# Performance work log

Hardware: AMD Instinct MI355X
Metric: run time of the kernel (lower is better)

## Reference

```python
import jax, jax.numpy as jnp
import numpy as np

L, B, IN, H, OUT = 4, 4096, 1024, 1024, 1024


def setup_inputs() -> dict:
    key = jax.random.key(0)
    ks = jax.random.split(key, 9)
    std = 1.0 / (H + IN) ** 0.5
    return {
        "x": jax.random.normal(ks[0], (B, IN), jnp.float32),
        "h_prev": jax.random.normal(ks[1], (L, B, H), jnp.float32),
        "c_prev": jax.random.normal(ks[2], (L, B, H), jnp.float32),
        "Wi": jax.random.uniform(ks[3], (L, IN, 4 * H), jnp.float32, -std, std),
        "Wh": jax.random.uniform(ks[4], (L, H, 4 * H), jnp.float32, -std, std),
        "bi": jax.random.uniform(ks[5], (L, 4 * H), jnp.float32, -std, std),
        "bh": jax.random.uniform(ks[6], (L, 4 * H), jnp.float32, -std, std),
        "fc_W": jax.random.uniform(ks[7], (H, OUT), jnp.float32, -std, std),
        "fc_b": jax.random.uniform(ks[8], (OUT,), jnp.float32, -std, std),
    }


def _lstm_cell(x, h, c, Wi, Wh, bi, bh):
    # gates: [B, 4H], split into (input, forget, cell, output)
    gates = x @ Wi + bi + h @ Wh + bh
    i, f, g, o = jnp.split(gates, 4, axis=1)
    i, f, o = jax.nn.sigmoid(i), jax.nn.sigmoid(f), jax.nn.sigmoid(o)
    g = jnp.tanh(g)
    c_cur = f * c + i * g
    h_cur = o * jnp.tanh(c_cur)
    return h_cur, c_cur


def reference(x, h_prev, c_prev, Wi, Wh, bi, bh, fc_W, fc_b):
    h_out, c_out = [], []
    x_in = x
    for l in range(L):  # fixed small layer loop
        h_cur, c_cur = _lstm_cell(x_in, h_prev[l], c_prev[l], Wi[l], Wh[l], bi[l], bh[l])
        h_out.append(h_cur)
        c_out.append(c_cur)
        x_in = h_cur
    h_out = jnp.stack(h_out, axis=0)
    c_out = jnp.stack(c_out, axis=0)
    y = h_out[-1] @ fc_W + fc_b
    return y, h_out, c_out
```

## Files before the change

kernel.cpp:

```cpp
#include <hip/hip_runtime.h>

#define B_    4096
#define H_    1024
#define NLAY  4
#define NK    32
#define NT512 512

typedef __attribute__((ext_vector_type(8))) short bf16x8;
typedef __attribute__((ext_vector_type(4))) float f32x4;
typedef unsigned short ushort_t;

__device__ __forceinline__ ushort_t f2bf(float f) {
  unsigned u = __builtin_bit_cast(unsigned, f);
  u += 0x7FFFu + ((u >> 16) & 1u);
  return (ushort_t)(u >> 16);
}

__device__ __forceinline__ float fast_sigmoid(float x) {
  float e = __expf(-fabsf(x));
  float s = 1.0f / (1.0f + e);
  return x >= 0.0f ? s : 1.0f - s;
}
__device__ __forceinline__ float fast_tanh(float x) {
  float e = __expf(-2.0f * fabsf(x));
  float t = (1.0f - e) / (1.0f + e);
  return x >= 0.0f ? t : -t;
}

#define GLDS16(gsrc, ldst)                                                  \
  __builtin_amdgcn_global_load_lds(                                         \
      (__attribute__((address_space(1))) void*)(gsrc),                      \
      (__attribute__((address_space(3))) void*)(ldst), 16, 0, 0)

#define BAR()                                                               \
  { asm volatile("" ::: "memory");                                          \
    __builtin_amdgcn_s_barrier();                                           \
    asm volatile("" ::: "memory"); }

#define WAITV(N)                                                            \
  { asm volatile("s_waitcnt vmcnt(" #N ")" ::: "memory");                   \
    __builtin_amdgcn_sched_barrier(0); }

__global__ __launch_bounds__(NT512, 2) void lstm8(
    const ushort_t* __restrict__ aX, const ushort_t* __restrict__ aH,
    const float* __restrict__ cprev, const float* __restrict__ bi,
    const float* __restrict__ bh, const ushort_t* __restrict__ wt,
    float* __restrict__ hout, float* __restrict__ cout,
    ushort_t* __restrict__ hbfout) {
  __shared__ __align__(16) char sL[131072];

  const int tid  = threadIdx.x;
  const int lane = tid & 63;
  const int wid  = tid >> 6;
  const int wm   = wid >> 2;
  const int wn   = wid & 3;
  const int bid  = (blockIdx.x & 7) * 32 + (blockIdx.x >> 3);
  const int bm   = bid & 15;
  const int bn   = bid >> 4;

  const int fr    = lane & 15;
  const int oF    = lane >> 4;
  const int s_    = oF ^ ((fr >> 1) & 3);
  const int aBase = (wm * 128 + fr) * 64 + s_ * 16;
  const int bBase = (wn * 64 + fr) * 64 + s_ * 16;

  const int rA = tid >> 2;
  const int oA = (tid & 3) ^ ((rA >> 1) & 3);
  const size_t aOff = (size_t)(bm * 256 + rA) * 1024 + oA * 8;

  f32x4 acc[8][4];
#pragma unroll
  for (int m = 0; m < 8; ++m)
#pragma unroll
    for (int g = 0; g < 4; ++g) acc[m][g] = (f32x4){0.f, 0.f, 0.f, 0.f};

#define STAGE_A(nb, kt, kh)                                                  \
  {                                                                          \
    const ushort_t* s0 =                                                     \
        (((kt) < 16) ? aX : aH) + aOff + ((kt) & 15) * 64 + (kh) * 32;       \
    GLDS16(s0, sL + (nb)*65536 + (kh)*16384 + wid * 1024);                   \
    GLDS16(s0 + 131072, sL + (nb)*65536 + (kh)*16384 + 8192 + wid * 1024);   \
  }
#define STAGE_B(nb, kt, kh)                                                  \
  {                                                                          \
    const ushort_t* s0 =                                                     \
        wt + ((size_t)(bn * 32 + (kt))) * 16384 + (kh)*8192 + tid * 8;       \
    GLDS16(s0, sL + (nb)*65536 + 32768 + (kh)*16384 + wid * 1024);           \
    GLDS16(s0 + 4096,                                                        \
           sL + (nb)*65536 + 32768 + (kh)*16384 + 8192 + wid * 1024);        \
  }

  STAGE_A(0, 0, 0);
  STAGE_B(0, 0, 0);
  STAGE_A(0, 0, 1);
  STAGE_B(0, 0, 1);
  WAITV(4);
  BAR();

#pragma unroll 1
  for (int kt = 0; kt < NK; ++kt) {
    const int cb = kt & 1, nb = cb ^ 1;
    const bool st = (kt + 1 < NK);
    const char* pa = sL + cb * 65536;
    const char* pb = sL + cb * 65536 + 32768;

    bf16x8 a[8], bb0, bb1;
#pragma unroll
    for (int m = 0; m < 8; ++m)
      a[m] = *(const bf16x8*)(pa + aBase + m * 1024);
    bb0 = *(const bf16x8*)(pb + bBase);
    bb1 = *(const bf16x8*)(pb + bBase + 1024);
    if (st) STAGE_A(nb, kt + 1, 0);
    BAR();
    __builtin_amdgcn_s_setprio(1);
#pragma unroll
    for (int m = 0; m < 8; ++m)
      acc[m][0] = __builtin_amdgcn_mfma_f32_16x16x32_bf16(a[m], bb0, acc[m][0], 0, 0, 0);
#pragma unroll
    for (int m = 0; m < 8; ++m)
      acc[m][1] = __builtin_amdgcn_mfma_f32_16x16x32_bf16(a[m], bb1, acc[m][1], 0, 0, 0);
    __builtin_amdgcn_s_setprio(0);
    BAR();
    bb0 = *(const bf16x8*)(pb + bBase + 2048);
    bb1 = *(const bf16x8*)(pb + bBase + 3072);
    if (st) STAGE_B(nb, kt + 1, 0);
    BAR();
    __builtin_amdgcn_s_setprio(1);
#pragma unroll
    for (int m = 0; m < 8; ++m)
      acc[m][2] = __builtin_amdgcn_mfma_f32_16x16x32_bf16(a[m], bb0, acc[m][2], 0, 0, 0);
#pragma unroll
    for (int m = 0; m < 8; ++m)
      acc[m][3] = __builtin_amdgcn_mfma_f32_16x16x32_bf16(a[m], bb1, acc[m][3], 0, 0, 0);
    __builtin_amdgcn_s_setprio(0);
    if (st) { WAITV(4); } else { WAITV(0); }
    BAR();
#pragma unroll
    for (int m = 0; m < 8; ++m)
      a[m] = *(const bf16x8*)(pa + 16384 + aBase + m * 1024);
    bb0 = *(const bf16x8*)(pb + 16384 + bBase);
    bb1 = *(const bf16x8*)(pb + 16384 + bBase + 1024);
    if (st) STAGE_A(nb, kt + 1, 1);
    BAR();
    __builtin_amdgcn_s_setprio(1);
#pragma unroll
    for (int m = 0; m < 8; ++m)
      acc[m][0] = __builtin_amdgcn_mfma_f32_16x16x32_bf16(a[m], bb0, acc[m][0], 0, 0, 0);
#pragma unroll
    for (int m = 0; m < 8; ++m)
      acc[m][1] = __builtin_amdgcn_mfma_f32_16x16x32_bf16(a[m], bb1, acc[m][1], 0, 0, 0);
    __builtin_amdgcn_s_setprio(0);
    BAR();
    bb0 = *(const bf16x8*)(pb + 16384 + bBase + 2048);
    bb1 = *(const bf16x8*)(pb + 16384 + bBase + 3072);
    if (st) STAGE_B(nb, kt + 1, 1);
    BAR();
    __builtin_amdgcn_s_setprio(1);
#pragma unroll
    for (int m = 0; m < 8; ++m)
      acc[m][2] = __builtin_amdgcn_mfma_f32_16x16x32_bf16(a[m], bb0, acc[m][2], 0, 0, 0);
#pragma unroll
    for (int m = 0; m < 8; ++m)
      acc[m][3] = __builtin_amdgcn_mfma_f32_16x16x32_bf16(a[m], bb1, acc[m][3], 0, 0, 0);
    __builtin_amdgcn_s_setprio(0);
    if (st) { WAITV(4); }
    BAR();
  }
#undef STAGE_A
#undef STAGE_B

  const int hcol = bn * 64 + wn * 16 + fr;
  float bsum[4];
#pragma unroll
  for (int g = 0; g < 4; ++g)
    bsum[g] = bi[g * 1024 + hcol] + bh[g * 1024 + hcol];
#pragma unroll
  for (int m = 0; m < 8; ++m) {
    const int row0 = bm * 256 + wm * 128 + m * 16 + (lane >> 4) * 4;
#pragma unroll
    for (int r = 0; r < 4; ++r) {
      const int row = row0 + r;
      const float gi = fast_sigmoid(acc[m][0][r] + bsum[0]);
      const float gf = fast_sigmoid(acc[m][1][r] + bsum[1]);
      const float gg = fast_tanh(acc[m][2][r] + bsum[2]);
      const float go = fast_sigmoid(acc[m][3][r] + bsum[3]);
      const float cp = cprev[(size_t)row * H_ + hcol];
      const float c  = gf * cp + gi * gg;
      const float h  = go * fast_tanh(c);
      cout[(size_t)row * H_ + hcol]   = c;
      hout[(size_t)row * H_ + hcol]   = h;
      hbfout[(size_t)row * H_ + hcol] = f2bf(h);
    }
  }
}

__global__ __launch_bounds__(NT512) void packW(const float* __restrict__ Wi,
                                               const float* __restrict__ Wh,
                                               ushort_t* __restrict__ wt) {
  __shared__ ushort_t t16[64 * 256];
  const int bn = blockIdx.x;
  const int ks = blockIdx.y;
  const int l  = blockIdx.z;
  const int tid = threadIdx.x;
  const int kq = tid >> 6, cc = tid & 63;
  const int k0 = ks * 64;
  const float* W = (k0 < 1024)
                       ? (Wi + (size_t)l * 1024 * 4096 + (size_t)k0 * 4096)
                       : (Wh + (size_t)l * 1024 * 4096 + (size_t)(k0 - 1024) * 4096);
#pragma unroll
  for (int kk = 0; kk < 8; ++kk) {
    const int kl = kq * 8 + kk;
#pragma unroll
    for (int g = 0; g < 4; ++g) {
      const float v = W[(size_t)kl * 4096 + g * 1024 + bn * 64 + cc];
      const int p = (cc >> 4) * 64 + g * 16 + (cc & 15);
      t16[kl * 256 + p] = f2bf(v);
    }
  }
  __syncthreads();
  ushort_t* tile = wt + (((size_t)l * 16 + bn) * 32 + ks) * 16384;
#pragma unroll
  for (int j = 0; j < 4; ++j) {
    const int idx = j * 512 + tid;
    const int q = idx & 1023;
    const int r = q >> 2, s = q & 3;
    const int o = s ^ ((r >> 1) & 3);
    const int kl = (idx >> 10) * 32 + o * 8;
    bf16x8 ov;
#pragma unroll
    for (int i = 0; i < 8; ++i) ov[i] = (short)t16[(kl + i) * 256 + r];
    *(bf16x8*)(tile + (size_t)idx * 8) = ov;
  }
}

__device__ __forceinline__ int swz(int row, int kelem) {
  return ((row * 64 + kelem) * 2) ^ ((row & 7) << 4);
}

__global__ __launch_bounds__(NT512) void fc_kernel(
    const ushort_t* __restrict__ wtfc, const ushort_t* __restrict__ abf,
    const float* __restrict__ bias, float* __restrict__ y) {
  __shared__ __align__(16) char sA[128 * 64 * 2];
  __shared__ __align__(16) char sB[64 * 64 * 2];
  const int tid  = threadIdx.x;
  const int lane = tid & 63;
  const int wid  = tid >> 6;
  const int wm   = wid >> 2;
  const int wn   = wid & 3;
  const int bid  = (blockIdx.x & 7) * 64 + (blockIdx.x >> 3);
  const int bm   = bid & 31;
  const int bn   = bid >> 5;

  f32x4 acc[4];
#pragma unroll
  for (int m = 0; m < 4; ++m) acc[m] = (f32x4){0.f, 0.f, 0.f, 0.f};

  const int rloc = wid * 8 + (lane >> 3);
  const int jA   = (lane & 7) ^ ((lane >> 3) & 7);
  const ushort_t* aSrc = abf + (size_t)(bm * 128 + rloc) * 1024 + jA * 8;

  for (int ks = 0; ks < 16; ++ks) {
    __syncthreads();
    GLDS16(wtfc + (size_t)(bn * 16 + ks) * 4096 + tid * 8, sB + wid * 1024);
    const int off = ks * 64;
    GLDS16(aSrc + off,             sA + wid * 1024);
    GLDS16(aSrc + off + 64 * 1024, sA + 8192 + wid * 1024);
    __syncthreads();
#pragma unroll
    for (int kk = 0; kk < 64; kk += 32) {
      const int ke = kk + (lane >> 4) * 8;
      bf16x8 a[4];
#pragma unroll
      for (int m = 0; m < 4; ++m)
        a[m] = *(const bf16x8*)(sA + swz(wm * 64 + m * 16 + (lane & 15), ke));
      bf16x8 b = *(const bf16x8*)(sB + swz(wn * 16 + (lane & 15), ke));
#pragma unroll
      for (int m = 0; m < 4; ++m)
        acc[m] = __builtin_amdgcn_mfma_f32_16x16x32_bf16(a[m], b, acc[m], 0, 0, 0);
    }
  }
  const int col = bn * 64 + wn * 16 + (lane & 15);
  const float bb = bias[col];
#pragma unroll
  for (int m = 0; m < 4; ++m) {
    const int row0 = bm * 128 + wm * 64 + m * 16 + ((lane >> 4) << 2);
#pragma unroll
    for (int r = 0; r < 4; ++r)
      y[(size_t)(row0 + r) * 1024 + col] = acc[m][r] + bb;
  }
}

__global__ __launch_bounds__(NT512) void transposeFc(const float* __restrict__ W,
                                                     ushort_t* __restrict__ wt) {
  const int bn = blockIdx.x;
  const int ks = blockIdx.y;
  const int tid = threadIdx.x;
  const int c  = tid & 63;
  const int ko = (tid >> 6) * 8;
  float v[8];
#pragma unroll
  for (int j = 0; j < 8; ++j)
    v[j] = W[(size_t)(ks * 64 + ko + j) * 1024 + bn * 64 + c];
  bf16x8 o;
#pragma unroll
  for (int j = 0; j < 8; ++j) o[j] = (short)f2bf(v[j]);
  ushort_t* tile = wt + ((size_t)bn * 16 + ks) * 4096;
  *(bf16x8*)((char*)tile + swz(c, ko)) = o;
}

__global__ __launch_bounds__(256) void cvt_bf16(const float* __restrict__ s,
                                                ushort_t* __restrict__ d,
                                                int n8) {
  const int i = blockIdx.x * 256 + threadIdx.x;
  if (i >= n8) return;
  const float* p = s + (size_t)i * 8;
  f32x4 a = ((const f32x4*)p)[0];
  f32x4 b = ((const f32x4*)p)[1];
  bf16x8 o;
#pragma unroll
  for (int j = 0; j < 4; ++j) {
    o[j]     = (short)f2bf(a[j]);
    o[4 + j] = (short)f2bf(b[j]);
  }
  *(bf16x8*)(d + (size_t)i * 8) = o;
}

extern "C" void kernel_launch(void* const* d_in, const int* in_sizes, int n_in,
                              void* d_out, int out_size, void* d_ws,
                              size_t ws_size, hipStream_t stream) {
  const float* x     = (const float*)d_in[0];
  const float* hprev = (const float*)d_in[1];
  const float* cprev = (const float*)d_in[2];
  const float* Wi    = (const float*)d_in[3];
  const float* Wh    = (const float*)d_in[4];
  const float* bi    = (const float*)d_in[5];
  const float* bh    = (const float*)d_in[6];
  const float* fcW   = (const float*)d_in[7];
  const float* fcb   = (const float*)d_in[8];

  float* out = (float*)d_out;
  const size_t BH = (size_t)B_ * H_;
  float* y    = out;
  float* hout = out + BH;
  float* cout = out + 5 * BH;

  const size_t WT_ELEMS = (size_t)4 * 16 * 32 * 16384;
  const size_t FC_ELEMS = (size_t)16 * 16 * 4096;
  ushort_t* wt      = (ushort_t*)d_ws;
  ushort_t* fcwt    = wt + WT_ELEMS;
  ushort_t* xbf     = fcwt + FC_ELEMS;
  ushort_t* hprevbf = xbf + BH;
  ushort_t* houtbf  = hprevbf + 4 * BH;

  dim3 blk(NT512);
  packW<<<dim3(16, 32, 4), blk, 0, stream>>>(Wi, Wh, wt);
  transposeFc<<<dim3(16, 16), blk, 0, stream>>>(fcW, fcwt);
  cvt_bf16<<<dim3((int)(BH / 8 / 256)), dim3(256), 0, stream>>>(x, xbf,
                                                                (int)(BH / 8));
  cvt_bf16<<<dim3((int)(4 * BH / 8 / 256)), dim3(256), 0, stream>>>(
      hprev, hprevbf, (int)(4 * BH / 8));

  for (int l = 0; l < NLAY; ++l) {
    const ushort_t* aX  = (l == 0) ? xbf : (houtbf + (size_t)(l - 1) * BH);
    const ushort_t* wtl = wt + (size_t)l * 16 * 32 * 16384;
    lstm8<<<dim3(256), blk, 0, stream>>>(
        aX, hprevbf + (size_t)l * BH, cprev + (size_t)l * BH, bi + l * 4096,
        bh + l * 4096, wtl, hout + (size_t)l * BH, cout + (size_t)l * BH,
        houtbf + (size_t)l * BH);
  }
  fc_kernel<<<dim3(512), blk, 0, stream>>>(fcwt, houtbf + 3 * BH, fcb, y);
}
```

Baseline: 434.2 us.

## Use 4-buffer 3-deep LDS pipeline and coalesce LSTM epilogue via LDS

The LSTM GEMM main loop moves from a double-buffered pipeline over 64-wide K tiles, which had several barriers per half-step, to a four-slot ring of 32-wide K tiles prefetched three steps ahead with a single wait and barrier per step. The packed weight layout is split into 8192-element half tiles to match. The epilogue now stages c_prev, c and h through LDS so global reads and writes are coalesced float4 rows, with the bf16 h copy written as 4-wide vectors. The cost is extra LDS round trips and barriers in the epilogue, and the deeper prefetch may raise register and LDS pressure.

```diff
diff --git a/kernel.cpp b/kernel.cpp
--- a/kernel.cpp
+++ b/kernel.cpp
@@ -3,10 +3,10 @@
 #define B_    4096
 #define H_    1024
 #define NLAY  4
-#define NK    32
 #define NT512 512
 
 typedef __attribute__((ext_vector_type(8))) short bf16x8;
+typedef __attribute__((ext_vector_type(4))) short s16x4;
 typedef __attribute__((ext_vector_type(4))) float f32x4;
 typedef unsigned short ushort_t;
 
@@ -68,130 +68,164 @@
   const int oA = (tid & 3) ^ ((rA >> 1) & 3);
   const size_t aOff = (size_t)(bm * 256 + rA) * 1024 + oA * 8;
 
+  const ushort_t* wtBn = wt + (size_t)bn * 64 * 8192;
+
   f32x4 acc[8][4];
 #pragma unroll
   for (int m = 0; m < 8; ++m)
 #pragma unroll
     for (int g = 0; g < 4; ++g) acc[m][g] = (f32x4){0.f, 0.f, 0.f, 0.f};
 
-#define STAGE_A(nb, kt, kh)                                                  \
+#pragma unroll
+  for (int t = 0; t < 3; ++t) {
+    const ushort_t* s0 = aX + aOff + t * 32;
+    GLDS16(s0,          sL + t * 32768 + wid * 1024);
+    GLDS16(s0 + 131072, sL + t * 32768 + 8192 + wid * 1024);
+    const ushort_t* sb = wtBn + (size_t)t * 8192 + tid * 8;
+    GLDS16(sb,        sL + t * 32768 + 16384 + wid * 1024);
+    GLDS16(sb + 4096, sL + t * 32768 + 16384 + 8192 + wid * 1024);
+  }
+  WAITV(8);
+  BAR();
+
+#define TSTEP(BUFC, T, ISSUE)                                                \
   {                                                                          \
-    const ushort_t* s0 =                                                     \
-        (((kt) < 16) ? aX : aH) + aOff + ((kt) & 15) * 64 + (kh) * 32;       \
-    GLDS16(s0, sL + (nb)*65536 + (kh)*16384 + wid * 1024);                   \
-    GLDS16(s0 + 131072, sL + (nb)*65536 + (kh)*16384 + 8192 + wid * 1024);   \
-  }
-#define STAGE_B(nb, kt, kh)                                                  \
-  {                                                                          \
-    const ushort_t* s0 =                                                     \
-        wt + ((size_t)(bn * 32 + (kt))) * 16384 + (kh)*8192 + tid * 8;       \
-    GLDS16(s0, sL + (nb)*65536 + 32768 + (kh)*16384 + wid * 1024);           \
-    GLDS16(s0 + 4096,                                                        \
-           sL + (nb)*65536 + 32768 + (kh)*16384 + 8192 + wid * 1024);        \
-  }
-
-  STAGE_A(0, 0, 0);
-  STAGE_B(0, 0, 0);
-  STAGE_A(0, 0, 1);
-  STAGE_B(0, 0, 1);
-  WAITV(4);
-  BAR();
+    const char* pa = sL + (BUFC) * 32768;                                    \
+    const char* pb = pa + 16384;                                             \
+    char* nbuf = sL + (((BUFC) + 3) & 3) * 32768;                            \
+    bf16x8 a[8], b0, b1;                                                     \
+    _Pragma("unroll")                                                        \
+    for (int m = 0; m < 8; ++m)                                              \
+      a[m] = *(const bf16x8*)(pa + aBase + m * 1024);                        \
+    b0 = *(const bf16x8*)(pb + bBase);                                       \
+    b1 = *(const bf16x8*)(pb + bBase + 1024);                                \
+    if (ISSUE) {                                                             \
+      const int tt = (T) + 3;                                                \
+      const ushort_t* s0 = (tt < 32 ? aX : aH) + (aOff + (tt & 31) * 32);    \
+      GLDS16(s0,          nbuf + wid * 1024);                                \
+      GLDS16(s0 + 131072, nbuf + 8192 + wid * 1024);                         \
+    }                                                                        \
+    __builtin_amdgcn_s_setprio(1);                                           \
+    _Pragma("unroll")                                                        \
+    for (int m = 0; m < 8; ++m)                                              \
+      acc[m][0] =                                                            \
+          __builtin_amdgcn_mfma_f32_16x16x32_bf16(a[m], b0, acc[m][0], 0, 0, 0); \
+    _Pragma("unroll")                                                        \
+    for (int m = 0; m < 8; ++m)                                              \
+      acc[m][1] =                                                            \
+          __builtin_amdgcn_mfma_f32_16x16x32_bf16(a[m], b1, acc[m][1], 0, 0, 0); \
+    __builtin_amdgcn_s_setprio(0);                                           \
+    bf16x8 b2 = *(const bf16x8*)(pb + bBase + 2048);                         \
+    bf16x8 b3 = *(const bf16x8*)(pb + bBase + 3072);                         \
+    if (ISSUE) {                                                             \
+      const int tt = (T) + 3;                                                \
+      const ushort_t* sb = wtBn + (size_t)tt * 8192 + tid * 8;               \
+      GLDS16(sb,        nbuf + 16384 + wid * 1024);                          \
+      GLDS16(sb + 4096, nbuf + 16384 + 8192 + wid * 1024);                   \
+    }                                                                        \
+    __builtin_amdgcn_s_setprio(1);                                           \
+    _Pragma("unroll")                                                        \
+    for (int m = 0; m < 8; ++m)                                              \
+      acc[m][2] =                                                            \
+          __builtin_amdgcn_mfma_f32_16x16x32_bf16(a[m], b2, acc[m][2], 0, 0, 0); \
+    _Pragma("unroll")                                                        \
+    for (int m = 0; m < 8; ++m)                                              \
+      acc[m][3] =                                                            \
+          __builtin_amdgcn_mfma_f32_16x16x32_bf16(a[m], b3, acc[m][3], 0, 0, 0); \
+    __builtin_amdgcn_s_setprio(0);                                           \
+  }
 
 #pragma unroll 1
-  for (int kt = 0; kt < NK; ++kt) {
-    const int cb = kt & 1, nb = cb ^ 1;
-    const bool st = (kt + 1 < NK);
-    const char* pa = sL + cb * 65536;
-    const char* pb = sL + cb * 65536 + 32768;
-
-    bf16x8 a[8], bb0, bb1;
-#pragma unroll
-    for (int m = 0; m < 8; ++m)
-      a[m] = *(const bf16x8*)(pa + aBase + m * 1024);
-    bb0 = *(const bf16x8*)(pb + bBase);
-    bb1 = *(const bf16x8*)(pb + bBase + 1024);
-    if (st) STAGE_A(nb, kt + 1, 0);
-    BAR();
-    __builtin_amdgcn_s_setprio(1);
-#pragma unroll
-    for (int m = 0; m < 8; ++m)
-      acc[m][0] = __builtin_amdgcn_mfma_f32_16x16x32_bf16(a[m], bb0, acc[m][0], 0, 0, 0);
-#pragma unroll
-    for (int m = 0; m < 8; ++m)
-      acc[m][1] = __builtin_amdgcn_mfma_f32_16x16x32_bf16(a[m], bb1, acc[m][1], 0, 0, 0);
-    __builtin_amdgcn_s_setprio(0);
-    BAR();
-    bb0 = *(const bf16x8*)(pb + bBase + 2048);
-    bb1 = *(const bf16x8*)(pb + bBase + 3072);
-    if (st) STAGE_B(nb, kt + 1, 0);
-    BAR();
-    __builtin_amdgcn_s_setprio(1);
-#pragma unroll
-    for (int m = 0; m < 8; ++m)
-      acc[m][2] = __builtin_amdgcn_mfma_f32_16x16x32_bf16(a[m], bb0, acc[m][2], 0, 0, 0);
-#pragma unroll
-    for (int m = 0; m < 8; ++m)
-      acc[m][3] = __builtin_amdgcn_mfma_f32_16x16x32_bf16(a[m], bb1, acc[m][3], 0, 0, 0);
-    __builtin_amdgcn_s_setprio(0);
-    if (st) { WAITV(4); } else { WAITV(0); }
-    BAR();
-#pragma unroll
-    for (int m = 0; m < 8; ++m)
-      a[m] = *(const bf16x8*)(pa + 16384 + aBase + m * 1024);
-    bb0 = *(const bf16x8*)(pb + 16384 + bBase);
-    bb1 = *(const bf16x8*)(pb + 16384 + bBase + 1024);
-    if (st) STAGE_A(nb, kt + 1, 1);
-    BAR();
-    __builtin_amdgcn_s_setprio(1);
-#pragma unroll
-    for (int m = 0; m < 8; ++m)
-      acc[m][0] = __builtin_amdgcn_mfma_f32_16x16x32_bf16(a[m], bb0, acc[m][0], 0, 0, 0);
-#pragma unroll
-    for (int m = 0; m < 8; ++m)
-      acc[m][1] = __builtin_amdgcn_mfma_f32_16x16x32_bf16(a[m], bb1, acc[m][1], 0, 0, 0);
-    __builtin_amdgcn_s_setprio(0);
-    BAR();
-    bb0 = *(const bf16x8*)(pb + 16384 + bBase + 2048);
-    bb1 = *(const bf16x8*)(pb + 16384 + bBase + 3072);
-    if (st) STAGE_B(nb, kt + 1, 1);
-    BAR();
-    __builtin_amdgcn_s_setprio(1);
-#pragma unroll
-    for (int m = 0; m < 8; ++m)
-      acc[m][2] = __builtin_amdgcn_mfma_f32_16x16x32_bf16(a[m], bb0, acc[m][2], 0, 0, 0);
-#pragma unroll
-    for (int m = 0; m < 8; ++m)
-      acc[m][3] = __builtin_amdgcn_mfma_f32_16x16x32_bf16(a[m], bb1, acc[m][3], 0, 0, 0);
-    __builtin_amdgcn_s_setprio(0);
-    if (st) { WAITV(4); }
-    BAR();
-  }
-#undef STAGE_A
-#undef STAGE_B
-
-  const int hcol = bn * 64 + wn * 16 + fr;
+  for (int t = 0; t < 60; t += 4) {
+    TSTEP(0, t + 0, 1) WAITV(8); BAR();
+    TSTEP(1, t + 1, 1) WAITV(8); BAR();
+    TSTEP(2, t + 2, 1) WAITV(8); BAR();
+    TSTEP(3, t + 3, 1) WAITV(8); BAR();
+  }
+  TSTEP(0, 60, 1) WAITV(8); BAR();
+  TSTEP(1, 61, 0) WAITV(4); BAR();
+  TSTEP(2, 62, 0) WAITV(0); BAR();
+  TSTEP(3, 63, 0)
+#undef TSTEP
+
+  const int hcolL = wn * 16 + fr;
+  const int hcol  = bn * 64 + hcolL;
   float bsum[4];
 #pragma unroll
   for (int g = 0; g < 4; ++g)
     bsum[g] = bi[g * 1024 + hcol] + bh[g * 1024 + hcol];
+
+#define LSTRIDE 68
+  float* LF = (float*)sL;
+  const int crow = (tid >> 4);
+  const int cc4  = (tid & 15) * 4;
+  BAR();
+  {
+    const float* cp0 = cprev + (size_t)(bm * 256) * 1024 + bn * 64;
+#pragma unroll
+    for (int i = 0; i < 8; ++i) {
+      const int row = i * 32 + crow;
+      f32x4 v = *(const f32x4*)(cp0 + (size_t)row * 1024 + cc4);
+      *(f32x4*)(LF + row * LSTRIDE + cc4) = v;
+    }
+  }
+  BAR();
+  float cv[8][4], hv[8][4];
 #pragma unroll
   for (int m = 0; m < 8; ++m) {
-    const int row0 = bm * 256 + wm * 128 + m * 16 + (lane >> 4) * 4;
+    const int rowb = wm * 128 + m * 16 + oF * 4;
 #pragma unroll
     for (int r = 0; r < 4; ++r) {
-      const int row = row0 + r;
+      const float cp = LF[(rowb + r) * LSTRIDE + hcolL];
       const float gi = fast_sigmoid(acc[m][0][r] + bsum[0]);
       const float gf = fast_sigmoid(acc[m][1][r] + bsum[1]);
       const float gg = fast_tanh(acc[m][2][r] + bsum[2]);
       const float go = fast_sigmoid(acc[m][3][r] + bsum[3]);
-      const float cp = cprev[(size_t)row * H_ + hcol];
       const float c  = gf * cp + gi * gg;
-      const float h  = go * fast_tanh(c);
-      cout[(size_t)row * H_ + hcol]   = c;
-      hout[(size_t)row * H_ + hcol]   = h;
-      hbfout[(size_t)row * H_ + hcol] = f2bf(h);
-    }
-  }
+      cv[m][r] = c;
+      hv[m][r] = go * fast_tanh(c);
+    }
+  }
+  BAR();
+#pragma unroll
+  for (int m = 0; m < 8; ++m) {
+    const int rowb = wm * 128 + m * 16 + oF * 4;
+#pragma unroll
+    for (int r = 0; r < 4; ++r) LF[(rowb + r) * LSTRIDE + hcolL] = cv[m][r];
+  }
+  BAR();
+  {
+    float* co0 = cout + (size_t)(bm * 256) * 1024 + bn * 64;
+#pragma unroll
+    for (int i = 0; i < 8; ++i) {
+      const int row = i * 32 + crow;
+      f32x4 v = *(const f32x4*)(LF + row * LSTRIDE + cc4);
+      *(f32x4*)(co0 + (size_t)row * 1024 + cc4) = v;
+    }
+  }
+  BAR();
+#pragma unroll
+  for (int m = 0; m < 8; ++m) {
+    const int rowb = wm * 128 + m * 16 + oF * 4;
+#pragma unroll
+    for (int r = 0; r < 4; ++r) LF[(rowb + r) * LSTRIDE + hcolL] = hv[m][r];
+  }
+  BAR();
+  {
+    float* ho0 = hout + (size_t)(bm * 256) * 1024 + bn * 64;
+    ushort_t* hb0 = hbfout + (size_t)(bm * 256) * 1024 + bn * 64;
+#pragma unroll
+    for (int i = 0; i < 8; ++i) {
+      const int row = i * 32 + crow;
+      f32x4 v = *(const f32x4*)(LF + row * LSTRIDE + cc4);
+      *(f32x4*)(ho0 + (size_t)row * 1024 + cc4) = v;
+      s16x4 hb;
+#pragma unroll
+      for (int j = 0; j < 4; ++j) hb[j] = (short)f2bf(v[j]);
+      *(s16x4*)(hb0 + (size_t)row * 1024 + cc4) = hb;
+    }
+  }
+#undef LSTRIDE
 }
 
 __global__ __launch_bounds__(NT512) void packW(const float* __restrict__ Wi,
@@ -199,11 +233,11 @@
                                                ushort_t* __restrict__ wt) {
   __shared__ ushort_t t16[64 * 256];
   const int bn = blockIdx.x;
-  const int ks = blockIdx.y;
+  const int kb = blockIdx.y;
   const int l  = blockIdx.z;
   const int tid = threadIdx.x;
   const int kq = tid >> 6, cc = tid & 63;
-  const int k0 = ks * 64;
+  const int k0 = kb * 64;
   const float* W = (k0 < 1024)
                        ? (Wi + (size_t)l * 1024 * 4096 + (size_t)k0 * 4096)
                        : (Wh + (size_t)l * 1024 * 4096 + (size_t)(k0 - 1024) * 4096);
@@ -218,18 +252,21 @@
     }
   }
   __syncthreads();
-  ushort_t* tile = wt + (((size_t)l * 16 + bn) * 32 + ks) * 16384;
-#pragma unroll
-  for (int j = 0; j < 4; ++j) {
-    const int idx = j * 512 + tid;
-    const int q = idx & 1023;
-    const int r = q >> 2, s = q & 3;
-    const int o = s ^ ((r >> 1) & 3);
-    const int kl = (idx >> 10) * 32 + o * 8;
-    bf16x8 ov;
-#pragma unroll
-    for (int i = 0; i < 8; ++i) ov[i] = (short)t16[(kl + i) * 256 + r];
-    *(bf16x8*)(tile + (size_t)idx * 8) = ov;
+#pragma unroll
+  for (int half = 0; half < 2; ++half) {
+    ushort_t* tile =
+        wt + (((size_t)l * 16 + bn) * 64 + kb * 2 + half) * 8192;
+#pragma unroll
+    for (int j = 0; j < 2; ++j) {
+      const int q = j * 512 + tid;
+      const int r = q >> 2, s = q & 3;
+      const int o = s ^ ((r >> 1) & 3);
+      const int kl = half * 32 + o * 8;
+      bf16x8 ov;
+#pragma unroll
+      for (int i = 0; i < 8; ++i) ov[i] = (short)t16[(kl + i) * 256 + r];
+      *(bf16x8*)(tile + (size_t)q * 8) = ov;
+    }
   }
 }
 
@@ -344,7 +381,7 @@
   float* hout = out + BH;
   float* cout = out + 5 * BH;
 
-  const size_t WT_ELEMS = (size_t)4 * 16 * 32 * 16384;
+  const size_t WT_ELEMS = (size_t)4 * 16 * 64 * 8192;
   const size_t FC_ELEMS = (size_t)16 * 16 * 4096;
   ushort_t* wt      = (ushort_t*)d_ws;
   ushort_t* fcwt    = wt + WT_ELEMS;
@@ -362,7 +399,7 @@
 
   for (int l = 0; l < NLAY; ++l) {
     const ushort_t* aX  = (l == 0) ? xbf : (houtbf + (size_t)(l - 1) * BH);
-    const ushort_t* wtl = wt + (size_t)l * 16 * 32 * 16384;
+    const ushort_t* wtl = wt + (size_t)l * 16 * 64 * 8192;
     lstm8<<<dim3(256), blk, 0, stream>>>(
         aX, hprevbf + (size_t)l * BH, cprev + (size_t)l * BH, bi + l * 4096,
         bh + l * 4096, wtl, hout + (size_t)l * BH, cout + (size_t)l * BH,
```

Result: faster. 391.6 us (-9.8%).
